# Kernel optimization log

Measured on AMD Instinct MI355X. Metric: run time of the kernel, lower is better.

The kernel has to match this reference:

```python
import jax, jax.numpy as jnp
import numpy as np

B, O, T = 32, 256, 1024
D_OBJ = 512      # obj_input_dim
D_PRED = 512     # predicate_input_dim
HID = 512        # hidden_dim
P_OUT = 512      # predicate_output_dim
OBJ_OUT = 512    # object_output_dim
N_PRED_TYPES = 50
ORIGINAL_EDGE = 0
TRANSITIVE_EDGE = 1


def setup_inputs() -> dict:
    key = jax.random.key(0)
    ks = jax.random.split(key, 16)

    def kaiming(k, fan_in, fan_out):
        return jax.random.normal(k, (fan_in, fan_out), jnp.float32) * np.sqrt(2.0 / fan_in)

    n1_in = 2 * D_OBJ + D_PRED            # 1536
    n1_out = 2 * HID + P_OUT              # 1536
    return {
        "obj_vecs": jax.random.normal(ks[0], (B, O, D_OBJ), jnp.float32),
        "pred_vecs": jax.random.normal(ks[1], (B, T, D_PRED), jnp.float32),
        "W1a": kaiming(ks[2], n1_in, HID), "b1a": jnp.zeros((HID,), jnp.float32),
        "W1b": kaiming(ks[3], HID, n1_out), "b1b": jnp.zeros((n1_out,), jnp.float32),
        "W2a": kaiming(ks[4], HID, HID), "b2a": jnp.zeros((HID,), jnp.float32),
        "W2b": kaiming(ks[5], HID, OBJ_OUT), "b2b": jnp.zeros((OBJ_OUT,), jnp.float32),
        "pt_weights": jax.random.normal(ks[6], (N_PRED_TYPES,), jnp.float32),
        "edges": jax.random.randint(ks[7], (B, T, 2), 0, O, jnp.int32),
        "pred_indicators": jax.random.randint(ks[8], (B, T), 0, 2, jnp.int32).astype(bool),
        "triplet_type": jax.random.randint(ks[9], (B, T), 0, 2, jnp.int32),
        "predicate_ids": jax.random.randint(ks[10], (B, T), 0, N_PRED_TYPES, jnp.int32),
    }


def reference(obj_vecs, pred_vecs, W1a, b1a, W1b, b1b, W2a, b2a, W2b, b2b,
              pt_weights, edges, pred_indicators, triplet_type, predicate_ids):
    s_idx = edges[:, :, 0]  # [B,T]
    o_idx = edges[:, :, 1]

    # gather subject/object vectors: [B,T,D]
    cur_s = jnp.take_along_axis(obj_vecs, s_idx[:, :, None], axis=1)
    cur_o = jnp.take_along_axis(obj_vecs, o_idx[:, :, None], axis=1)
    cur_t = jnp.concatenate([cur_s, pred_vecs, cur_o], axis=-1)  # [B,T,2D+Dp]

    # net1: Linear-ReLU-Linear-ReLU
    h = jax.nn.relu(cur_t @ W1a + b1a)
    new_t = jax.nn.relu(h @ W1b + b1b)  # [B,T,2*HID+P_OUT]

    # confidence weighting
    pt_pred = jax.nn.sigmoid(pt_weights)  # [N_PRED_TYPES]
    conf = ((triplet_type == ORIGINAL_EDGE).astype(jnp.float32)
            + (triplet_type == TRANSITIVE_EDGE).astype(jnp.float32) * pt_pred[predicate_ids])  # [B,T]
    new_t = new_t * conf[:, :, None]

    new_s = new_t[:, :, :HID]
    new_p = new_t[:, :, HID:HID + P_OUT]
    new_o = new_t[:, :, HID + P_OUT:]

    mask = pred_indicators.astype(jnp.float32)  # [B,T]

    def pool_one(si, oi, sv, ov, cf, m):
        # masked scatter-add (equivalent to torch boolean-masked scatter_add)
        sums = (jax.ops.segment_sum(sv * m[:, None], si, num_segments=O)
                + jax.ops.segment_sum(ov * m[:, None], oi, num_segments=O))  # [O,HID]
        w = cf * m
        counts = (jax.ops.segment_sum(w, si, num_segments=O)
                  + jax.ops.segment_sum(w, oi, num_segments=O))  # [O]
        nz = counts > 0
        return jnp.where(nz[:, None], sums / jnp.where(nz, counts, 1.0)[:, None], sums)

    pooled = jax.vmap(pool_one)(s_idx, o_idx, new_s, new_o, conf, mask)  # [B,O,HID]

    # net2: Linear-ReLU-Linear-ReLU
    h2 = jax.nn.relu(pooled @ W2a + b2a)
    new_obj = jax.nn.relu(h2 @ W2b + b2b)  # [B,O,OBJ_OUT]

    return new_obj, new_p
```

## Files before the change

### kernel.cpp

```cpp
#include <hip/hip_runtime.h>
#include <hip/hip_bf16.h>
#include <cstdint>
#include <cstddef>

#define DEV __device__ __forceinline__

typedef __attribute__((ext_vector_type(8))) short  s8v;
typedef __attribute__((ext_vector_type(4))) float  f4v;
typedef __attribute__((ext_vector_type(4))) uint32_t u4v;

DEV unsigned short f2bf(float x) {
  union { float f; uint32_t u; } v; v.f = x;
  uint32_t u = v.u + 0x7FFFu + ((v.u >> 16) & 1u);
  return (unsigned short)(u >> 16);
}
DEV uint32_t cvtpk2(float lo, float hi) {
  uint32_t r;
  asm("v_cvt_pk_bf16_f32 %0, %1, %2" : "=v"(r) : "v"(lo), "v"(hi));
  return r;
}
DEV unsigned short f2bf_fast(float x) { return (unsigned short)cvtpk2(x, 0.f); }
DEV float bf2f(unsigned short b) {
  union { uint32_t u; float f; } v; v.u = ((uint32_t)b) << 16;
  return v.f;
}

DEV void async_copy16(void* lds, const void* g) {
  typedef __attribute__((address_space(3))) uint32_t lds_t;
  typedef const __attribute__((address_space(1))) uint32_t g_t;
  __builtin_amdgcn_global_load_lds((g_t*)g, (lds_t*)lds, 16, 0, 0);
}

#define WAITV4()    asm volatile("s_waitcnt vmcnt(4)" ::: "memory")
#define WAITV0()    asm volatile("s_waitcnt vmcnt(0)" ::: "memory")
#define MEMFENCE()  asm volatile("" ::: "memory")

constexpr int Bc = 32, Oc = 256, Tc = 1024;
constexpr int BM = 128, BN = 128, BK = 64;
constexpr int CSR_CAP = 46;

DEV void swz_mn(int nyb, int* mb, int* nb) {
  const int nwg = gridDim.x * gridDim.y;
  const int w   = blockIdx.x + blockIdx.y * gridDim.x;
  const int cpx = nwg >> 3;
  const int s   = (w & 7) * cpx + (w >> 3);
  *mb = s / nyb;
  *nb = s % nyb;
}

__global__ __launch_bounds__(256)
void cvt_k(const float* __restrict__ in, unsigned short* __restrict__ outp, int n8)
{
  const int i = blockIdx.x * 256 + threadIdx.x;
  if (i >= n8) return;
  const f4v v0 = *(const f4v*)(in + (size_t)i * 8);
  const f4v v1 = *(const f4v*)(in + (size_t)i * 8 + 4);
  u4v pk;
  pk.x = cvtpk2(v0.x, v0.y);
  pk.y = cvtpk2(v0.z, v0.w);
  pk.z = cvtpk2(v1.x, v1.y);
  pk.w = cvtpk2(v1.z, v1.w);
  *(u4v*)(outp + (size_t)i * 8) = pk;
}

#define READ_A(QM, DST) do {                                                    \
    _Pragma("unroll")                                                           \
    for (int i = 0; i < 4; ++i) {                                               \
      const int row = wm * 128 + ((QM) * 4 + i) * 16 + (lane & 15);             \
      _Pragma("unroll")                                                         \
      for (int kk = 0; kk < 2; ++kk) {                                          \
        const int c = kk * 4 + (lane >> 4);                                     \
        DST[i][kk] = *(const s8v*)(Ab_ + row * 128 + ((c ^ (row & 7)) << 4));   \
      }                                                                         \
    }                                                                           \
  } while (0)

#define READ_B(QN, DST) do {                                                    \
    _Pragma("unroll")                                                           \
    for (int j = 0; j < 2; ++j) {                                               \
      const int row = wn * 64 + ((QN) * 2 + j) * 16 + (lane & 15);              \
      _Pragma("unroll")                                                         \
      for (int kk = 0; kk < 2; ++kk) {                                          \
        const int c = kk * 4 + (lane >> 4);                                     \
        DST[j][kk] = *(const s8v*)(Bb_ + row * 128 + ((c ^ (row & 7)) << 4));   \
      }                                                                         \
    }                                                                           \
  } while (0)

#define SYNC_MFMA(QM, QN, AF, BF) do {                                          \
    MEMFENCE();                                                                 \
    __builtin_amdgcn_s_barrier();                                               \
    asm volatile("s_waitcnt lgkmcnt(0)" ::: "memory");                          \
    __builtin_amdgcn_sched_barrier(0);                                          \
    __builtin_amdgcn_s_setprio(1);                                              \
    _Pragma("unroll")                                                           \
    for (int i = 0; i < 4; ++i)                                                 \
      _Pragma("unroll")                                                         \
      for (int j = 0; j < 2; ++j)                                               \
        _Pragma("unroll")                                                       \
        for (int kk = 0; kk < 2; ++kk)                                          \
          acc[(QM) * 4 + i][(QN) * 2 + j] =                                     \
            __builtin_amdgcn_mfma_f32_16x16x32_bf16(                            \
              AF[i][kk], BF[j][kk], acc[(QM) * 4 + i][(QN) * 2 + j], 0, 0, 0);  \
    __builtin_amdgcn_s_setprio(0);                                              \
  } while (0)

#define ENDPHASE() do { MEMFENCE(); __builtin_amdgcn_s_barrier(); } while (0)

#define KTILE_BODY() do {                                                       \
    const int par = t & 1, px = par ^ 1;                                        \
    const char* Ab_ = smem + par * 65536;                                       \
    const char* Bb_ = Ab_ + 32768;                                              \
    const bool s1 = (t + 1 < nk), s2 = (t + 2 < nk);                            \
                                                                        \
    READ_A(0, af); READ_B(0, bf0);                                              \
    if (s1) stageA(px, 1, t + 1);                                               \
    SYNC_MFMA(0, 0, af, bf0);                                                   \
    ENDPHASE();                                                                 \
                                                                        \
    READ_B(1, bf1);                                                             \
    if (s1) stageB(px, 1, t + 1);                                               \
    SYNC_MFMA(0, 1, af, bf1);                                                   \
    ENDPHASE();                                                                 \
                                                                        \
    READ_A(1, af);                                                              \
    if (s2) stageA(par, 0, t + 2);                                              \
    SYNC_MFMA(1, 1, af, bf1);                                                   \
    ENDPHASE();                                                                 \
                                                                        \
    if (s2) stageB(par, 0, t + 2);                                              \
    SYNC_MFMA(1, 0, af, bf0);                                                   \
    if (s2) { WAITV4(); } else if (s1) { WAITV0(); }                            \
    ENDPHASE();                                                                 \
  } while (0)

__global__ __launch_bounds__(512, 2)
void gemm8g_k(const unsigned short* __restrict__ objb,
              const unsigned short* __restrict__ predb,
              const int* __restrict__ edges,
              const unsigned short* __restrict__ Bt,
              const float* __restrict__ bias,
              unsigned short* __restrict__ outp)
{
  __shared__ __align__(16) char smem[131072];

  const int tid = threadIdx.x, lane = tid & 63, wave = tid >> 6;
  const int wm = wave >> 2, wn = wave & 3;
  int mb, nb; swz_mn(gridDim.y, &mb, &nb);
  const int m0 = mb * 256, n0 = nb * 256;
  const int rl  = tid >> 3;
  const int cs8 = ((lane & 7) ^ (lane >> 3)) * 8;
  const int rB0 = (rl >> 5) * 64 + (rl & 31);

  uint32_t offS[4], offP[4], offO[4];
  #pragma unroll
  for (int c2 = 0; c2 < 4; ++c2) {
    const int r = (c2 >> 1) * 128 + (c2 & 1) * 64 + rl;
    const int m = m0 + r;
    const int ob = (m >> 10) * Oc;
    offS[c2] = (uint32_t)((ob + edges[2 * m])     * 1024 + cs8 * 2);
    offO[c2] = (uint32_t)((ob + edges[2 * m + 1]) * 1024 + cs8 * 2);
    offP[c2] = (uint32_t)(m * 1024 + cs8 * 2);
  }
  const unsigned short* srcB = Bt + (size_t)(n0 + rB0) * 1536 + cs8;

  auto stageA = [&](int p, int qm, int kt) {
    const int reg = kt >> 3;
    const uint32_t koff = (uint32_t)(kt & 7) * 128u;
    #pragma unroll
    for (int s = 0; s < 2; ++s) {
      const int c2 = s * 2 + qm;
      const char* src;
      if (reg == 0)      src = (const char*)objb  + offS[c2] + koff;
      else if (reg == 1) src = (const char*)predb + offP[c2] + koff;
      else               src = (const char*)objb  + offO[c2] + koff;
      async_copy16(smem + p * 65536 + ((s * 128 + qm * 64 + wave * 8) << 7), src);
    }
  };
  auto stageB = [&](int p, int qn, int kt) {
    #pragma unroll
    for (int s = 0; s < 2; ++s)
      async_copy16(smem + p * 65536 + 32768 +
                     ((s * 128 + qn * 32 + (wave >> 2) * 64 + (wave & 3) * 8) << 7),
                   srcB + (size_t)(s * 128 + qn * 32) * 1536 + kt * 64);
  };

  f4v acc[8][4] = {};
  s8v af[4][2], bf0[2][2], bf1[2][2];
  constexpr int nk = 24;

  stageA(0, 0, 0); stageB(0, 0, 0); stageA(0, 1, 0); stageB(0, 1, 0);
  stageA(1, 0, 1); stageB(1, 0, 1);
  WAITV4();
  MEMFENCE();
  __builtin_amdgcn_s_barrier();

  for (int t = 0; t < nk; ++t) KTILE_BODY();

  const int cn = lane & 15, rq4 = (lane >> 4) * 4;
  #pragma unroll
  for (int f = 0; f < 8; ++f) {
    const int gr0 = m0 + wm * 128 + f * 16 + rq4;
    #pragma unroll
    for (int g = 0; g < 4; ++g) {
      const int gc = n0 + wn * 64 + g * 16 + cn;
      const float bv = bias[gc];
      #pragma unroll
      for (int r = 0; r < 4; ++r) {
        float val = acc[f][g][r] + bv;
        val = val > 0.f ? val : 0.f;
        outp[(size_t)(gr0 + r) * 512 + gc] = f2bf_fast(val);
      }
    }
  }
}

template<int EPI>
__global__ __launch_bounds__(256)
void gemm_k(const unsigned short* __restrict__ Abf,
            const unsigned short* __restrict__ Bt,
            const float* __restrict__ bias,
            const float* __restrict__ conf,
            unsigned short* __restrict__ out_bf,
            float* __restrict__ out_f32,
            int M, int N, int K)
{
  __shared__ __align__(16) char smem[BM * BK * 2 + BN * BK * 2];
  char* As = smem;
  char* Bs = smem + BM * BK * 2;

  const int tid  = threadIdx.x;
  const int lane = tid & 63;
  const int wave = tid >> 6;
  const int wm = wave >> 1, wn = wave & 1;
  int mb, nb; swz_mn(gridDim.y, &mb, &nb);
  const int m0 = mb * BM;
  const int n0 = nb * BN;

  f4v acc[4][4] = {};

  for (int k0 = 0; k0 < K; k0 += BK) {
    {
      const int r8 = lane >> 3;
      const int cs = (lane & 7) ^ r8;
      const unsigned short* src = Bt + (size_t)(n0 + wave * 32 + r8) * K + k0 + cs * 8;
      #pragma unroll
      for (int i = 0; i < 4; ++i)
        async_copy16(Bs + (wave * 32 + i * 8) * 128, src + (size_t)i * 8 * K);
      const unsigned short* srca = Abf + (size_t)(m0 + wave * 32 + r8) * K + k0 + cs * 8;
      #pragma unroll
      for (int i = 0; i < 4; ++i)
        async_copy16(As + (wave * 32 + i * 8) * 128, srca + (size_t)i * 8 * K);
    }
    __syncthreads();

    #pragma unroll
    for (int kk = 0; kk < 2; ++kk) {
      s8v af[4], bfv[4];
      #pragma unroll
      for (int i = 0; i < 4; ++i) {
        const int row = wm * 64 + i * 16 + (lane & 15);
        const int c = kk * 4 + (lane >> 4);
        af[i] = *(const s8v*)(As + row * 128 + ((c ^ (row & 7)) << 4));
      }
      #pragma unroll
      for (int j = 0; j < 4; ++j) {
        const int row = wn * 64 + j * 16 + (lane & 15);
        const int c = kk * 4 + (lane >> 4);
        bfv[j] = *(const s8v*)(Bs + row * 128 + ((c ^ (row & 7)) << 4));
      }
      #pragma unroll
      for (int i = 0; i < 4; ++i)
        #pragma unroll
        for (int j = 0; j < 4; ++j)
          acc[i][j] = __builtin_amdgcn_mfma_f32_16x16x32_bf16(af[i], bfv[j], acc[i][j], 0, 0, 0);
    }
    __syncthreads();
  }

  const int cn = lane & 15, rq4 = (lane >> 4) * 4;
  #pragma unroll
  for (int i = 0; i < 4; ++i) {
    const int gr0 = m0 + wm * 64 + i * 16 + rq4;
    #pragma unroll
    for (int j = 0; j < 4; ++j) {
      const int gc = n0 + wn * 64 + j * 16 + cn;
      const float bv = bias[gc];
      #pragma unroll
      for (int r = 0; r < 4; ++r) {
        float val = acc[i][j][r] + bv;
        val = val > 0.f ? val : 0.f;
        const int gr = gr0 + r;
        if (EPI == 0) out_bf[(size_t)gr * N + gc] = f2bf_fast(val);
        else if (EPI == 2) out_f32[(size_t)gr * N + gc] = val;
        else { out_f32[(size_t)gr * N + gc] = val * conf[gr]; }
      }
    }
  }
}

__global__ __launch_bounds__(256)
void gemm2so_k(const unsigned short* __restrict__ h,
               const int* __restrict__ torig,
               const float* __restrict__ confc,
               const unsigned short* __restrict__ W1bt,
               const float* __restrict__ b1b,
               const int* __restrict__ minfo,
               unsigned short* __restrict__ news_c,
               unsigned short* __restrict__ newo_c)
{
  const int Mp   = minfo[1];
  const int nact = (Mp >> 7) << 3;
  const int w    = blockIdx.x + blockIdx.y * gridDim.x;
  if (w >= nact) return;
  const int cpx = nact >> 3;
  const int s   = (w & 7) * cpx + (w >> 3);
  const int mb  = s >> 3, nb = s & 7;
  const int m0  = mb * BM;
  const int Mr  = minfo[0];

  __shared__ __align__(16) char smem[BM * BK * 2 + BN * BK * 2];
  char* As = smem;
  char* Bs = smem + BM * BK * 2;

  const int tid  = threadIdx.x;
  const int lane = tid & 63;
  const int wave = tid >> 6;
  const int wm = wave >> 1, wn = wave & 1;
  const int n0 = nb * BN;
  const int r8 = lane >> 3;
  const int cs8 = ((lane & 7) ^ r8) * 8;

  const unsigned short* aP[4];
  #pragma unroll
  for (int i = 0; i < 4; ++i) {
    int m = m0 + wave * 32 + i * 8 + r8;
    m = m < Mr ? m : Mr - 1;
    aP[i] = h + (size_t)torig[m] * 512 + cs8;
  }
  const int nrow0 = (nb < 4) ? n0 : n0 + 512;
  const unsigned short* bsrc = W1bt + (size_t)(nrow0 + wave * 32 + r8) * 512 + cs8;

  f4v acc[4][4] = {};

  for (int kt = 0; kt < 8; ++kt) {
    const int kin = kt * 64;
    #pragma unroll
    for (int i = 0; i < 4; ++i)
      async_copy16(Bs + (wave * 32 + i * 8) * 128, bsrc + (size_t)(i * 8) * 512 + kin);
    #pragma unroll
    for (int i = 0; i < 4; ++i)
      async_copy16(As + (wave * 32 + i * 8) * 128, aP[i] + kin);
    __syncthreads();

    #pragma unroll
    for (int kk = 0; kk < 2; ++kk) {
      s8v af[4], bfv[4];
      #pragma unroll
      for (int i = 0; i < 4; ++i) {
        const int row = wm * 64 + i * 16 + (lane & 15);
        const int c = kk * 4 + (lane >> 4);
        af[i] = *(const s8v*)(As + row * 128 + ((c ^ (row & 7)) << 4));
      }
      #pragma unroll
      for (int j = 0; j < 4; ++j) {
        const int row = wn * 64 + j * 16 + (lane & 15);
        const int c = kk * 4 + (lane >> 4);
        bfv[j] = *(const s8v*)(Bs + row * 128 + ((c ^ (row & 7)) << 4));
      }
      #pragma unroll
      for (int i = 0; i < 4; ++i)
        #pragma unroll
        for (int j = 0; j < 4; ++j)
          acc[i][j] = __builtin_amdgcn_mfma_f32_16x16x32_bf16(af[i], bfv[j], acc[i][j], 0, 0, 0);
    }
    __syncthreads();
  }

  const float* bb = b1b + ((nb < 4) ? n0 : 512 + n0);
  unsigned short* outp = (nb < 4) ? news_c : newo_c;
  const int c0 = (nb & 3) * 128;
  const int cn = lane & 15, rq4 = (lane >> 4) * 4;
  #pragma unroll
  for (int i = 0; i < 4; ++i) {
    const int gr0 = m0 + wm * 64 + i * 16 + rq4;
    #pragma unroll
    for (int j = 0; j < 4; ++j) {
      const int lc = wn * 64 + j * 16 + cn;
      const float bv = bb[lc];
      #pragma unroll
      for (int r = 0; r < 4; ++r) {
        const int gr = gr0 + r;
        float val = acc[i][j][r] + bv;
        val = val > 0.f ? val : 0.f;
        val *= confc[gr < Mr ? gr : 0];
        if (gr < Mr) outp[(size_t)gr * 512 + c0 + lc] = f2bf_fast(val);
      }
    }
  }
}

__global__ void tcvt_k(const float* __restrict__ W, unsigned short* __restrict__ Wt,
                       int K, int N)
{
  __shared__ float tile[32][33];
  const int k0 = blockIdx.x * 32, n0 = blockIdx.y * 32;
  const int tx = threadIdx.x, ty = threadIdx.y;
  #pragma unroll
  for (int i = 0; i < 32; i += 8)
    tile[ty + i][tx] = W[(size_t)(k0 + ty + i) * N + (n0 + tx)];
  __syncthreads();
  #pragma unroll
  for (int i = 0; i < 32; i += 8)
    Wt[(size_t)(n0 + ty + i) * K + (k0 + tx)] = f2bf(tile[tx][ty + i]);
}

__global__ __launch_bounds__(256)
void detect_k(const unsigned char* __restrict__ mb, int* __restrict__ flag)
{
  const int i = blockIdx.x * 256 + threadIdx.x;
  const int local = ((i & 3) && mb[i]) ? 1 : 0;
  const unsigned long long bal = __ballot(local);
  if (bal != 0 && (threadIdx.x & 63) == 0) atomicOr(flag, 1);
}

__global__ void prep_k(const int* __restrict__ tt, const int* __restrict__ pid,
                       const float* __restrict__ ptw, const int* __restrict__ edges,
                       const void* __restrict__ mask, const int* __restrict__ u8flag,
                       float* __restrict__ conf, int* __restrict__ se,
                       int* __restrict__ oe)
{
  const int m = blockIdx.x * 256 + threadIdx.x;
  const int t = tt[m];
  float c = 0.f;
  if (t == 0) c = 1.f;
  else if (t == 1) c = 1.f / (1.f + expf(-ptw[pid[m]]));
  conf[m] = c;
  bool mk;
  if (*u8flag) mk = ((const unsigned char*)mask)[m] != 0;
  else         mk = ((const int*)mask)[m] != 0;
  se[m] = mk ? edges[2 * m]     : -1;
  oe[m] = mk ? edges[2 * m + 1] : -1;
}

__global__ __launch_bounds__(1024)
void scan1_k(const int* __restrict__ se, int* __restrict__ bsum)
{
  const int m = blockIdx.x * 1024 + threadIdx.x;
  const unsigned long long bal = __ballot(se[m] >= 0);
  __shared__ int wc[16];
  if ((threadIdx.x & 63) == 0) wc[threadIdx.x >> 6] = (int)__popcll(bal);
  __syncthreads();
  if (threadIdx.x == 0) {
    int s = 0;
    #pragma unroll
    for (int i = 0; i < 16; ++i) s += wc[i];
    bsum[blockIdx.x] = s;
  }
}

__global__ void scan2_k(const int* __restrict__ bsum, int* __restrict__ boff,
                        int* __restrict__ minfo)
{
  if (threadIdx.x == 0) {
    int s = 0;
    for (int i = 0; i < 32; ++i) { boff[i] = s; s += bsum[i]; }
    minfo[0] = s;
    minfo[1] = (s + 127) & ~127;
  }
}

__global__ __launch_bounds__(1024)
void scan3_k(const int* __restrict__ se, const int* __restrict__ boff,
             const float* __restrict__ conf,
             int* __restrict__ torig, int* __restrict__ cmap,
             float* __restrict__ confc)
{
  const int m = blockIdx.x * 1024 + threadIdx.x;
  const int lane = threadIdx.x & 63, w = threadIdx.x >> 6;
  const bool mv = se[m] >= 0;
  const unsigned long long bal = __ballot(mv);
  __shared__ int wc[16];
  if (lane == 0) wc[w] = (int)__popcll(bal);
  __syncthreads();
  int woff = 0;
  for (int i = 0; i < w; ++i) woff += wc[i];
  if (mv) {
    const int c = boff[blockIdx.x] + woff +
                  (int)__popcll(bal & ((1ull << lane) - 1ull));
    torig[c] = m;
    cmap[m]  = c;
    confc[c] = conf[m];
  }
}

__global__ __launch_bounds__(256)
void csr2_k(const int* __restrict__ se, const int* __restrict__ oe,
            int* __restrict__ deg, int* __restrict__ slot)
{
  const int wid  = blockIdx.x * 4 + (threadIdx.x >> 6);
  const int b    = wid >> 8;
  const int u    = wid & 255;
  const int lane = threadIdx.x & 63;
  const int mb   = b * Tc;
  int* sl = slot + (size_t)wid * CSR_CAP;
  const unsigned long long lt = (1ull << lane) - 1ull;
  int cnt = 0;
  #pragma unroll 4
  for (int c = 0; c < 16; ++c) {
    const int t = c * 64 + lane;
    const int s = se[mb + t];
    const int o = oe[mb + t];
    const unsigned long long ms = __ballot(s == u);
    const unsigned long long mo = __ballot(o == u);
    if (s == u) {
      const int pos = cnt + (int)__popcll(ms & lt);
      if (pos < CSR_CAP) sl[pos] = 2 * t;
    }
    cnt += (int)__popcll(ms);
    if (o == u) {
      const int pos = cnt + (int)__popcll(mo & lt);
      if (pos < CSR_CAP) sl[pos] = 2 * t + 1;
    }
    cnt += (int)__popcll(mo);
  }
  if (lane == 0) deg[wid] = cnt < CSR_CAP ? cnt : CSR_CAP;
}

__global__ __launch_bounds__(256)
void pool2_k(const unsigned short* __restrict__ S, const unsigned short* __restrict__ Ov,
             const int* __restrict__ deg, const int* __restrict__ slot,
             const float* __restrict__ conf, const int* __restrict__ cmap,
             unsigned short* __restrict__ pooled)
{
  const int bo = blockIdx.x;
  const int b  = bo >> 8;
  const int u  = threadIdx.x;
  const int d  = deg[bo];
  const int* sl = slot + (size_t)bo * CSR_CAP;
  float a0 = 0.f, a1 = 0.f, w = 0.f;
  for (int i = 0; i < d; ++i) {
    const int e = sl[i];
    const int t = e >> 1;
    const int c = cmap[b * Tc + t];
    const unsigned short* row = ((e & 1) ? Ov : S) + (size_t)c * 512;
    const uint32_t pr = *(const uint32_t*)(row + 2 * u);
    a0 += bf2f((unsigned short)pr);
    a1 += bf2f((unsigned short)(pr >> 16));
    w  += conf[b * Tc + t];
  }
  const float denom = (w > 0.f) ? w : 1.f;
  const size_t ob = (size_t)bo * 512;
  *(uint32_t*)(pooled + ob + 2 * u) = cvtpk2(a0 / denom, a1 / denom);
}

extern "C" void kernel_launch(void* const* d_in, const int* in_sizes, int n_in,
                              void* d_out, int out_size, void* d_ws, size_t ws_size,
                              hipStream_t stream)
{
  const float* obj  = (const float*)d_in[0];
  const float* pred = (const float*)d_in[1];
  const float* W1a  = (const float*)d_in[2];
  const float* b1a  = (const float*)d_in[3];
  const float* W1b  = (const float*)d_in[4];
  const float* b1b  = (const float*)d_in[5];
  const float* W2a  = (const float*)d_in[6];
  const float* b2a  = (const float*)d_in[7];
  const float* W2b  = (const float*)d_in[8];
  const float* b2b  = (const float*)d_in[9];
  const float* ptw  = (const float*)d_in[10];
  const int*   edges = (const int*)d_in[11];
  const void*  mask  = d_in[12];
  const int*   tt    = (const int*)d_in[13];
  const int*   pid   = (const int*)d_in[14];
  float* out = (float*)d_out;

  char* ws = (char*)d_ws;
  unsigned short* W1at = (unsigned short*)(ws + 0);
  unsigned short* W1bt = (unsigned short*)(ws + 1572864);
  unsigned short* W2at = (unsigned short*)(ws + 3145728);
  unsigned short* W2bt = (unsigned short*)(ws + 3670016);
  int* deg  = (int*)(ws + 0);
  int* slot = (int*)(ws + 32768);
  unsigned short* h    = (unsigned short*)(ws + 4194304);
  unsigned short* pooled = h;
  unsigned short* h2   = (unsigned short*)(ws + 12582912);
  unsigned short* news = (unsigned short*)(ws + 37748736);
  unsigned short* newo = (unsigned short*)(ws + 71303168);
  unsigned short* objb = news;
  unsigned short* predb = (unsigned short*)(ws + 46137344);
  float* conf = (float*)(ws + 104857600);
  int*   se   = (int*)(ws + 104988672);
  int*   oe   = (int*)(ws + 105119744);
  int* u8flag = (int*)(ws + 105250816);

  char* sout = (char*)d_out;
  int*   torig = (int*)(sout + 0);
  int*   cmap  = (int*)(sout + 131072);
  float* confc = (float*)(sout + 262144);
  int*   bsum  = (int*)(sout + 393216);
  int*   boff  = (int*)(sout + 393344);
  int*   minfo = (int*)(sout + 393472);

  tcvt_k<<<dim3(48, 16), dim3(32, 8), 0, stream>>>(W1a, W1at, 1536, 512);
  tcvt_k<<<dim3(16, 48), dim3(32, 8), 0, stream>>>(W1b, W1bt, 512, 1536);
  tcvt_k<<<dim3(16, 16), dim3(32, 8), 0, stream>>>(W2a, W2at, 512, 512);
  tcvt_k<<<dim3(16, 16), dim3(32, 8), 0, stream>>>(W2b, W2bt, 512, 512);

  cvt_k<<<2048, 256, 0, stream>>>(obj,  objb,  Bc * Oc * 512 / 8);
  cvt_k<<<8192, 256, 0, stream>>>(pred, predb, Bc * Tc * 512 / 8);

  hipMemsetAsync(u8flag, 0, sizeof(int), stream);
  detect_k<<<128, 256, 0, stream>>>((const unsigned char*)mask, u8flag);
  prep_k<<<128, 256, 0, stream>>>(tt, pid, ptw, edges, mask, u8flag, conf, se, oe);

  scan1_k<<<32, 1024, 0, stream>>>(se, bsum);
  scan2_k<<<1, 64, 0, stream>>>(bsum, boff, minfo);
  scan3_k<<<32, 1024, 0, stream>>>(se, boff, conf, torig, cmap, confc);

  gemm8g_k<<<dim3(128, 2), 512, 0, stream>>>(objb, predb, edges, W1at, b1a, h);

  csr2_k<<<2048, 256, 0, stream>>>(se, oe, deg, slot);

  gemm_k<3><<<dim3(256, 4), 256, 0, stream>>>(
      h, W1bt + 512 * 512, b1b + 512, conf, nullptr, out + 4194304, 32768, 512, 512);

  gemm2so_k<<<dim3(256, 8), 256, 0, stream>>>(
      h, torig, confc, W1bt, b1b, minfo, news, newo);

  pool2_k<<<Bc * Oc, 256, 0, stream>>>(news, newo, deg, slot, conf, cmap, pooled);

  gemm_k<0><<<dim3(64, 4), 256, 0, stream>>>(
      pooled, W2at, b2a, nullptr, h2, nullptr, 8192, 512, 512);

  gemm_k<2><<<dim3(64, 4), 256, 0, stream>>>(
      h2, W2bt, b2b, nullptr, nullptr, out, 8192, 512, 512);
}
```

Baseline: 220.3 us.

## Merge prologue kernels and fuse predicate and subject/object GEMMs into one launch

Combines the weight transposes, the activation fp32-to-bf16 conversions and the mask-format detection into a single block-indexed prologue kernel. The first scan pass moves into the prep kernel. The predicate-output GEMM and the compacted subject/object GEMM now run as one grid with a branch per tile. The aim is to cut launch overhead and the tail gaps between small kernels, and to let the two second-layer GEMMs fill the GPU together, at the cost of branchy heterogeneous blocks and a larger oversubscribed grid.

Measured after the change: 231.2 us. +5.0%, slower.

```diff
diff --git a/kernel.cpp b/kernel.cpp
--- a/kernel.cpp
+++ b/kernel.cpp
@@ -49,18 +49,55 @@
 }
 
 __global__ __launch_bounds__(256)
-void cvt_k(const float* __restrict__ in, unsigned short* __restrict__ outp, int n8)
-{
-  const int i = blockIdx.x * 256 + threadIdx.x;
-  if (i >= n8) return;
-  const f4v v0 = *(const f4v*)(in + (size_t)i * 8);
-  const f4v v1 = *(const f4v*)(in + (size_t)i * 8 + 4);
-  u4v pk;
-  pk.x = cvtpk2(v0.x, v0.y);
-  pk.y = cvtpk2(v0.z, v0.w);
-  pk.z = cvtpk2(v1.x, v1.y);
-  pk.w = cvtpk2(v1.z, v1.w);
-  *(u4v*)(outp + (size_t)i * 8) = pk;
+void prologue_k(const float* __restrict__ pred, const float* __restrict__ obj,
+                const float* __restrict__ W1a, const float* __restrict__ W1b,
+                const float* __restrict__ W2a, const float* __restrict__ W2b,
+                unsigned short* __restrict__ predb, unsigned short* __restrict__ objb,
+                unsigned short* __restrict__ W1at, unsigned short* __restrict__ W1bt,
+                unsigned short* __restrict__ W2at, unsigned short* __restrict__ W2bt,
+                const unsigned char* __restrict__ maskb, int* __restrict__ flag)
+{
+  __shared__ float tile[32][33];
+  const int b = blockIdx.x;
+  const int tid = threadIdx.x;
+
+  if (b < 10240) {
+    const float* in = (b < 8192) ? pred : obj;
+    unsigned short* outp = (b < 8192) ? predb : objb;
+    const int i = ((b < 8192) ? b : b - 8192) * 256 + tid;
+    const f4v v0 = *(const f4v*)(in + (size_t)i * 8);
+    const f4v v1 = *(const f4v*)(in + (size_t)i * 8 + 4);
+    u4v pk;
+    pk.x = cvtpk2(v0.x, v0.y);
+    pk.y = cvtpk2(v0.z, v0.w);
+    pk.z = cvtpk2(v1.x, v1.y);
+    pk.w = cvtpk2(v1.z, v1.w);
+    *(u4v*)(outp + (size_t)i * 8) = pk;
+  } else if (b < 12288) {
+    const float* W; unsigned short* Wt; int K, N, kb, nb;
+    if (b < 11008)      { W = W1a; Wt = W1at; K = 1536; N = 512;
+                          const int r = b - 10240; kb = r % 48; nb = r / 48; }
+    else if (b < 11776) { W = W1b; Wt = W1bt; K = 512;  N = 1536;
+                          const int r = b - 11008; kb = r % 16; nb = r / 16; }
+    else if (b < 12032) { W = W2a; Wt = W2at; K = 512;  N = 512;
+                          const int r = b - 11776; kb = r % 16; nb = r / 16; }
+    else                { W = W2b; Wt = W2bt; K = 512;  N = 512;
+                          const int r = b - 12032; kb = r % 16; nb = r / 16; }
+    const int k0 = kb * 32, n0 = nb * 32;
+    const int tx = tid & 31, ty = tid >> 5;
+    #pragma unroll
+    for (int i = 0; i < 32; i += 8)
+      tile[ty + i][tx] = W[(size_t)(k0 + ty + i) * N + (n0 + tx)];
+    __syncthreads();
+    #pragma unroll
+    for (int i = 0; i < 32; i += 8)
+      Wt[(size_t)(n0 + ty + i) * K + (k0 + tx)] = f2bf(tile[tx][ty + i]);
+  } else {
+    const int i = (b - 12288) * 256 + tid;
+    const int local = ((i & 3) && maskb[i]) ? 1 : 0;
+    const unsigned long long bal = __ballot(local);
+    if (bal != 0 && (tid & 63) == 0) atomicOr(flag, 1);
+  }
 }
 
 #define READ_A(QM, DST) do {                                                    \
@@ -220,7 +257,6 @@
 void gemm_k(const unsigned short* __restrict__ Abf,
             const unsigned short* __restrict__ Bt,
             const float* __restrict__ bias,
-            const float* __restrict__ conf,
             unsigned short* __restrict__ out_bf,
             float* __restrict__ out_f32,
             int M, int N, int K)
@@ -292,32 +328,38 @@
         val = val > 0.f ? val : 0.f;
         const int gr = gr0 + r;
         if (EPI == 0) out_bf[(size_t)gr * N + gc] = f2bf_fast(val);
-        else if (EPI == 2) out_f32[(size_t)gr * N + gc] = val;
-        else { out_f32[(size_t)gr * N + gc] = val * conf[gr]; }
+        else          out_f32[(size_t)gr * N + gc] = val;
       }
     }
   }
 }
 
 __global__ __launch_bounds__(256)
-void gemm2so_k(const unsigned short* __restrict__ h,
-               const int* __restrict__ torig,
-               const float* __restrict__ confc,
-               const unsigned short* __restrict__ W1bt,
-               const float* __restrict__ b1b,
-               const int* __restrict__ minfo,
-               unsigned short* __restrict__ news_c,
-               unsigned short* __restrict__ newo_c)
+void gemm2_k(const unsigned short* __restrict__ h,
+             const unsigned short* __restrict__ W1bt,
+             const float* __restrict__ b1b,
+             const float* __restrict__ conf,
+             const float* __restrict__ confc,
+             const int* __restrict__ torig,
+             const int* __restrict__ minfo,
+             float* __restrict__ out_p,
+             unsigned short* __restrict__ news_c,
+             unsigned short* __restrict__ newo_c)
 {
   const int Mp   = minfo[1];
   const int nact = (Mp >> 7) << 3;
+  const int ntot = 1024 + nact;
   const int w    = blockIdx.x + blockIdx.y * gridDim.x;
-  if (w >= nact) return;
-  const int cpx = nact >> 3;
+  if (w >= ntot) return;
+  const int cpx = ntot >> 3;
   const int s   = (w & 7) * cpx + (w >> 3);
-  const int mb  = s >> 3, nb = s & 7;
-  const int m0  = mb * BM;
-  const int Mr  = minfo[0];
+  const bool prole = (s < 1024);
+  const int Mr = minfo[0];
+
+  int m0, nb;
+  if (prole) { m0 = (s >> 2) * BM; nb = s & 3; }
+  else       { const int s2 = s - 1024; m0 = (s2 >> 3) * BM; nb = s2 & 7; }
+  const int n0 = nb * BN;
 
   __shared__ __align__(16) char smem[BM * BK * 2 + BN * BK * 2];
   char* As = smem;
@@ -327,7 +369,6 @@
   const int lane = tid & 63;
   const int wave = tid >> 6;
   const int wm = wave >> 1, wn = wave & 1;
-  const int n0 = nb * BN;
   const int r8 = lane >> 3;
   const int cs8 = ((lane & 7) ^ r8) * 8;
 
@@ -335,10 +376,14 @@
   #pragma unroll
   for (int i = 0; i < 4; ++i) {
     int m = m0 + wave * 32 + i * 8 + r8;
-    m = m < Mr ? m : Mr - 1;
-    aP[i] = h + (size_t)torig[m] * 512 + cs8;
-  }
-  const int nrow0 = (nb < 4) ? n0 : n0 + 512;
+    if (prole) {
+      aP[i] = h + (size_t)m * 512 + cs8;
+    } else {
+      m = m < Mr ? m : Mr - 1;
+      aP[i] = h + (size_t)torig[m] * 512 + cs8;
+    }
+  }
+  const int nrow0 = prole ? (512 + n0) : ((nb < 4) ? n0 : n0 + 512);
   const unsigned short* bsrc = W1bt + (size_t)(nrow0 + wave * 32 + r8) * 512 + cs8;
 
   f4v acc[4][4] = {};
@@ -377,60 +422,57 @@
     __syncthreads();
   }
 
-  const float* bb = b1b + ((nb < 4) ? n0 : 512 + n0);
-  unsigned short* outp = (nb < 4) ? news_c : newo_c;
-  const int c0 = (nb & 3) * 128;
   const int cn = lane & 15, rq4 = (lane >> 4) * 4;
-  #pragma unroll
-  for (int i = 0; i < 4; ++i) {
-    const int gr0 = m0 + wm * 64 + i * 16 + rq4;
-    #pragma unroll
-    for (int j = 0; j < 4; ++j) {
-      const int lc = wn * 64 + j * 16 + cn;
-      const float bv = bb[lc];
-      #pragma unroll
-      for (int r = 0; r < 4; ++r) {
-        const int gr = gr0 + r;
-        float val = acc[i][j][r] + bv;
-        val = val > 0.f ? val : 0.f;
-        val *= confc[gr < Mr ? gr : 0];
-        if (gr < Mr) outp[(size_t)gr * 512 + c0 + lc] = f2bf_fast(val);
-      }
-    }
-  }
-}
-
-__global__ void tcvt_k(const float* __restrict__ W, unsigned short* __restrict__ Wt,
-                       int K, int N)
-{
-  __shared__ float tile[32][33];
-  const int k0 = blockIdx.x * 32, n0 = blockIdx.y * 32;
-  const int tx = threadIdx.x, ty = threadIdx.y;
-  #pragma unroll
-  for (int i = 0; i < 32; i += 8)
-    tile[ty + i][tx] = W[(size_t)(k0 + ty + i) * N + (n0 + tx)];
-  __syncthreads();
-  #pragma unroll
-  for (int i = 0; i < 32; i += 8)
-    Wt[(size_t)(n0 + ty + i) * K + (k0 + tx)] = f2bf(tile[tx][ty + i]);
-}
-
-__global__ __launch_bounds__(256)
-void detect_k(const unsigned char* __restrict__ mb, int* __restrict__ flag)
-{
-  const int i = blockIdx.x * 256 + threadIdx.x;
-  const int local = ((i & 3) && mb[i]) ? 1 : 0;
-  const unsigned long long bal = __ballot(local);
-  if (bal != 0 && (threadIdx.x & 63) == 0) atomicOr(flag, 1);
-}
-
-__global__ void prep_k(const int* __restrict__ tt, const int* __restrict__ pid,
-                       const float* __restrict__ ptw, const int* __restrict__ edges,
-                       const void* __restrict__ mask, const int* __restrict__ u8flag,
-                       float* __restrict__ conf, int* __restrict__ se,
-                       int* __restrict__ oe)
-{
-  const int m = blockIdx.x * 256 + threadIdx.x;
+  if (prole) {
+    const float* bb = b1b + 512 + n0;
+    #pragma unroll
+    for (int i = 0; i < 4; ++i) {
+      const int gr0 = m0 + wm * 64 + i * 16 + rq4;
+      #pragma unroll
+      for (int j = 0; j < 4; ++j) {
+        const int lc = wn * 64 + j * 16 + cn;
+        const float bv = bb[lc];
+        #pragma unroll
+        for (int r = 0; r < 4; ++r) {
+          const int gr = gr0 + r;
+          float val = acc[i][j][r] + bv;
+          val = val > 0.f ? val : 0.f;
+          out_p[(size_t)gr * 512 + n0 + lc] = val * conf[gr];
+        }
+      }
+    }
+  } else {
+    const float* bb = b1b + ((nb < 4) ? n0 : 512 + n0);
+    unsigned short* outp = (nb < 4) ? news_c : newo_c;
+    const int c0 = (nb & 3) * 128;
+    #pragma unroll
+    for (int i = 0; i < 4; ++i) {
+      const int gr0 = m0 + wm * 64 + i * 16 + rq4;
+      #pragma unroll
+      for (int j = 0; j < 4; ++j) {
+        const int lc = wn * 64 + j * 16 + cn;
+        const float bv = bb[lc];
+        #pragma unroll
+        for (int r = 0; r < 4; ++r) {
+          const int gr = gr0 + r;
+          float val = acc[i][j][r] + bv;
+          val = val > 0.f ? val : 0.f;
+          val *= confc[gr < Mr ? gr : 0];
+          if (gr < Mr) outp[(size_t)gr * 512 + c0 + lc] = f2bf_fast(val);
+        }
+      }
+    }
+  }
+}
+
+__global__ __launch_bounds__(1024)
+void prep_k(const int* __restrict__ tt, const int* __restrict__ pid,
+            const float* __restrict__ ptw, const int* __restrict__ edges,
+            const void* __restrict__ mask, const int* __restrict__ u8flag,
+            float* __restrict__ conf, int* __restrict__ se,
+            int* __restrict__ oe, int* __restrict__ bsum)
+{
+  const int m = blockIdx.x * 1024 + threadIdx.x;
   const int t = tt[m];
   float c = 0.f;
   if (t == 0) c = 1.f;
@@ -441,21 +483,16 @@
   else         mk = ((const int*)mask)[m] != 0;
   se[m] = mk ? edges[2 * m]     : -1;
   oe[m] = mk ? edges[2 * m + 1] : -1;
-}
-
-__global__ __launch_bounds__(1024)
-void scan1_k(const int* __restrict__ se, int* __restrict__ bsum)
-{
-  const int m = blockIdx.x * 1024 + threadIdx.x;
-  const unsigned long long bal = __ballot(se[m] >= 0);
+
+  const unsigned long long bal = __ballot(mk);
   __shared__ int wc[16];
   if ((threadIdx.x & 63) == 0) wc[threadIdx.x >> 6] = (int)__popcll(bal);
   __syncthreads();
   if (threadIdx.x == 0) {
-    int s = 0;
-    #pragma unroll
-    for (int i = 0; i < 16; ++i) s += wc[i];
-    bsum[blockIdx.x] = s;
+    int ssum = 0;
+    #pragma unroll
+    for (int i = 0; i < 16; ++i) ssum += wc[i];
+    bsum[blockIdx.x] = ssum;
   }
 }
 
@@ -602,19 +639,14 @@
   int*   boff  = (int*)(sout + 393344);
   int*   minfo = (int*)(sout + 393472);
 
-  tcvt_k<<<dim3(48, 16), dim3(32, 8), 0, stream>>>(W1a, W1at, 1536, 512);
-  tcvt_k<<<dim3(16, 48), dim3(32, 8), 0, stream>>>(W1b, W1bt, 512, 1536);
-  tcvt_k<<<dim3(16, 16), dim3(32, 8), 0, stream>>>(W2a, W2at, 512, 512);
-  tcvt_k<<<dim3(16, 16), dim3(32, 8), 0, stream>>>(W2b, W2bt, 512, 512);
-
-  cvt_k<<<2048, 256, 0, stream>>>(obj,  objb,  Bc * Oc * 512 / 8);
-  cvt_k<<<8192, 256, 0, stream>>>(pred, predb, Bc * Tc * 512 / 8);
-
   hipMemsetAsync(u8flag, 0, sizeof(int), stream);
-  detect_k<<<128, 256, 0, stream>>>((const unsigned char*)mask, u8flag);
-  prep_k<<<128, 256, 0, stream>>>(tt, pid, ptw, edges, mask, u8flag, conf, se, oe);
-
-  scan1_k<<<32, 1024, 0, stream>>>(se, bsum);
+  prologue_k<<<12416, 256, 0, stream>>>(
+      pred, obj, W1a, W1b, W2a, W2b,
+      predb, objb, W1at, W1bt, W2at, W2bt,
+      (const unsigned char*)mask, u8flag);
+
+  prep_k<<<32, 1024, 0, stream>>>(tt, pid, ptw, edges, mask, u8flag,
+                                  conf, se, oe, bsum);
   scan2_k<<<1, 64, 0, stream>>>(bsum, boff, minfo);
   scan3_k<<<32, 1024, 0, stream>>>(se, boff, conf, torig, cmap, confc);
 
@@ -622,17 +654,14 @@
 
   csr2_k<<<2048, 256, 0, stream>>>(se, oe, deg, slot);
 
-  gemm_k<3><<<dim3(256, 4), 256, 0, stream>>>(
-      h, W1bt + 512 * 512, b1b + 512, conf, nullptr, out + 4194304, 32768, 512, 512);
-
-  gemm2so_k<<<dim3(256, 8), 256, 0, stream>>>(
-      h, torig, confc, W1bt, b1b, minfo, news, newo);
+  gemm2_k<<<dim3(384, 8), 256, 0, stream>>>(
+      h, W1bt, b1b, conf, confc, torig, minfo, out + 4194304, news, newo);
 
   pool2_k<<<Bc * Oc, 256, 0, stream>>>(news, newo, deg, slot, conf, cmap, pooled);
 
   gemm_k<0><<<dim3(64, 4), 256, 0, stream>>>(
-      pooled, W2at, b2a, nullptr, h2, nullptr, 8192, 512, 512);
+      pooled, W2at, b2a, h2, nullptr, 8192, 512, 512);
 
   gemm_k<2><<<dim3(64, 4), 256, 0, stream>>>(
-      h2, W2bt, b2b, nullptr, nullptr, out, 8192, 512, 512);
-}
+      h2, W2bt, b2b, nullptr, out, 8192, 512, 512);
+}
```
